# Kernel optimization log

Hardware: AMD Instinct MI355X
Metric: run time of the kernel (lower is better)

## Reference

```python
import jax, jax.numpy as jnp
import numpy as np

LST = 64  # sparsemax frame length over time


def sparsemax(z):
    """Sparsemax over the last axis (Martins & Astudillo 2016)."""
    d = z.shape[-1]
    z_sorted = jnp.flip(jnp.sort(z, axis=-1), axis=-1)           # descending
    z_cumsum = jnp.cumsum(z_sorted, axis=-1)
    k = jnp.arange(1, d + 1, dtype=z.dtype)
    support = (1.0 + k * z_sorted) > z_cumsum                    # bool, [..., d]
    k_z = jnp.sum(support, axis=-1, keepdims=True)               # int, >=1
    tau_sum = jnp.take_along_axis(z_cumsum, k_z - 1, axis=-1)
    tau = (tau_sum - 1.0) / k_z.astype(z.dtype)
    return jnp.maximum(z - tau, 0.0)


def setup_inputs() -> dict:
    key = jax.random.key(0)
    midis_out = jax.random.normal(key, (16, 11, 65536), dtype=jnp.float32)
    return {"midis_out": midis_out}


def reference(midis_out):
    batch, n_insts, time = midis_out.shape
    lst = LST
    len_pad = (lst - time % lst) % lst
    x = jnp.pad(midis_out, ((0, 0), (0, 0), (0, len_pad)))
    t_pad = time + len_pad
    # sparsemax over instruments: (b, t, i) -> sparsemax over i -> back to (b, i, t)
    out_inst = jnp.swapaxes(sparsemax(jnp.swapaxes(x, 1, 2)), 1, 2)
    # sparsemax over fixed time blocks of length lst
    out_time = sparsemax(x.reshape(batch, n_insts, t_pad // lst, lst))
    out_time = out_time.reshape(batch, n_insts, t_pad)
    return out_inst[:, :, :time] * out_time[:, :, :time]
```

## Files before the change

### kernel.cpp

```cpp
#include <hip/hip_runtime.h>

#define B_   16
#define NI   11
#define T_   65536
#define LST  64
#define NBLK (T_ / LST)
#define ROWP 68

#define DPP_XOR1 0xB1
#define DPP_XOR2 0x4E

__device__ __forceinline__ float frcp(float x) { return __builtin_amdgcn_rcpf(x); }

template<int CTRL>
__device__ __forceinline__ float dppf(float x) {
    return __int_as_float(__builtin_amdgcn_update_dpp(
        0, __float_as_int(x), CTRL, 0xF, 0xF, true));
}
template<int CTRL>
__device__ __forceinline__ int dppi(int x) {
    return __builtin_amdgcn_update_dpp(0, x, CTRL, 0xF, 0xF, true);
}

__device__ __forceinline__ void ce_desc(float& a, float& b) {
    float mx = fmaxf(a, b);
    float mn = fminf(a, b);
    a = mx; b = mn;
}

__global__ __launch_bounds__(256) void fused_sparsemax_kernel(
        const float* __restrict__ in, float* __restrict__ out) {
    __shared__ float ldsz[4][NI * ROWP];
    __shared__ float ldsti[4][64];

    const int lane = threadIdx.x & 63;
    const int wid  = threadIdx.x >> 6;
    const int tile = blockIdx.x * 4 + wid;
    const int b    = tile >> 10;
    const int jb   = tile & (NBLK - 1);

    const float* px = in + (size_t)b * NI * T_ + (size_t)jb * LST + (size_t)lane;

    float z[NI];
#pragma unroll
    for (int i = 0; i < NI; ++i) z[i] = px[(size_t)i * T_];

#pragma unroll
    for (int i = 0; i < NI; ++i) ldsz[wid][i * ROWP + lane] = z[i];

    const int g   = lane >> 2;
    const int q   = lane & 3;
    const int row = (g < NI) ? g : (g - NI);

    float y[16];
#pragma unroll
    for (int r = 0; r < 16; ++r) y[r] = ldsz[wid][row * ROWP + q * 16 + r];

    float s[NI];
#pragma unroll
    for (int i = 0; i < NI; ++i) s[i] = z[i];
#pragma unroll
    for (int p = 0; p < NI; ++p) {
#pragma unroll
        for (int k = (p & 1); k + 1 < NI; k += 2) ce_desc(s[k], s[k + 1]);
    }
    float cum = 0.0f, tsum = 0.0f;
    int   kz  = 0;
#pragma unroll
    for (int k = 1; k <= NI; ++k) {
        cum += s[k - 1];
        bool cond = fmaf((float)k, s[k - 1], 1.0f) > cum;
        kz   += cond ? 1 : 0;
        tsum += cond ? s[k - 1] : 0.0f;
    }
    const float tau_i = (tsum - 1.0f) * frcp((float)kz);
    ldsti[wid][lane] = tau_i;

    float m = y[0];
#pragma unroll
    for (int r = 1; r < 16; ++r) m = fmaxf(m, y[r]);
    m = fmaxf(m, dppf<DPP_XOR1>(m));
    m = fmaxf(m, dppf<DPP_XOR2>(m));

    float tau  = m - 1.0f;
    int   prev = 0;
#pragma unroll
    for (int it = 0; it < 3; ++it) {
        float ss = 0.0f;
        int   cc = 0;
#pragma unroll
        for (int r = 0; r < 16; ++r) {
            bool a = y[r] > tau;
            ss += a ? y[r] : 0.0f;
            cc += a ? 1 : 0;
        }
        ss += dppf<DPP_XOR1>(ss);
        ss += dppf<DPP_XOR2>(ss);
        cc += dppi<DPP_XOR1>(cc);
        cc += dppi<DPP_XOR2>(cc);
        tau  = (ss - 1.0f) * frcp((float)cc);
        prev = cc;
    }
    for (int it = 0; it < LST; ++it) {
        float ss = 0.0f;
        int   cc = 0;
#pragma unroll
        for (int r = 0; r < 16; ++r) {
            bool a = y[r] > tau;
            ss += a ? y[r] : 0.0f;
            cc += a ? 1 : 0;
        }
        cc += dppi<DPP_XOR1>(cc);
        cc += dppi<DPP_XOR2>(cc);
        if (!__any(cc != prev)) break;
        ss += dppf<DPP_XOR1>(ss);
        ss += dppf<DPP_XOR2>(ss);
        prev = cc;
        tau  = (ss - 1.0f) * frcp((float)cc);
    }

    if (g < NI) {
        float ti[16];
#pragma unroll
        for (int r = 0; r < 16; ++r) ti[r] = ldsti[wid][q * 16 + r];

        float* po = out + (size_t)b * NI * T_ + (size_t)g * T_
                        + (size_t)jb * LST + (size_t)q * 16;
        float4* po4 = reinterpret_cast<float4*>(po);
#pragma unroll
        for (int v = 0; v < 4; ++v) {
            float4 o;
            o.x = fmaxf(y[4*v+0] - tau, 0.0f) * fmaxf(y[4*v+0] - ti[4*v+0], 0.0f);
            o.y = fmaxf(y[4*v+1] - tau, 0.0f) * fmaxf(y[4*v+1] - ti[4*v+1], 0.0f);
            o.z = fmaxf(y[4*v+2] - tau, 0.0f) * fmaxf(y[4*v+2] - ti[4*v+2], 0.0f);
            o.w = fmaxf(y[4*v+3] - tau, 0.0f) * fmaxf(y[4*v+3] - ti[4*v+3], 0.0f);
            po4[v] = o;
        }
    }
}

extern "C" void kernel_launch(void* const* d_in, const int* in_sizes, int n_in,
                              void* d_out, int out_size, void* d_ws, size_t ws_size,
                              hipStream_t stream) {
    const float* in = (const float*)d_in[0];
    float* out = (float*)d_out;
    hipLaunchKernelGGL(fused_sparsemax_kernel, dim3(4096), dim3(256), 0, stream,
                       in, out);
}
```

Baseline: 28.50 us.

## Restructure into 704-thread super-tiles with one wave per instrument row

Each block now handles 1024 time steps for all 11 instruments, with one wave per instrument row. Each lane loads 16 contiguous floats as float4 vectors, so no lanes sit idle (the old layout left 20 of 64 lanes unused in the store phase). The instrument-axis sparsemax is computed per column from a shared LDS tile across the whole block, and the time-block threshold starts from a tighter initial guess to cut iterations. The cost is block-wide syncthreads, 1024 large blocks that may limit occupancy, and a possible bank-conflict pattern when reading the LDS columns.

```diff
diff --git a/kernel.cpp b/kernel.cpp
--- a/kernel.cpp
+++ b/kernel.cpp
@@ -1,11 +1,11 @@
 #include <hip/hip_runtime.h>
 
-#define B_   16
-#define NI   11
-#define T_   65536
-#define LST  64
-#define NBLK (T_ / LST)
-#define ROWP 68
+#define B_    16
+#define NI    11
+#define T_    65536
+#define LST   64
+#define SUPER 1024
+#define RSTR  1040
 
 #define DPP_XOR1 0xB1
 #define DPP_XOR2 0x4E
@@ -28,37 +28,10 @@
     a = mx; b = mn;
 }
 
-__global__ __launch_bounds__(256) void fused_sparsemax_kernel(
-        const float* __restrict__ in, float* __restrict__ out) {
-    __shared__ float ldsz[4][NI * ROWP];
-    __shared__ float ldsti[4][64];
-
-    const int lane = threadIdx.x & 63;
-    const int wid  = threadIdx.x >> 6;
-    const int tile = blockIdx.x * 4 + wid;
-    const int b    = tile >> 10;
-    const int jb   = tile & (NBLK - 1);
-
-    const float* px = in + (size_t)b * NI * T_ + (size_t)jb * LST + (size_t)lane;
-
-    float z[NI];
-#pragma unroll
-    for (int i = 0; i < NI; ++i) z[i] = px[(size_t)i * T_];
-
-#pragma unroll
-    for (int i = 0; i < NI; ++i) ldsz[wid][i * ROWP + lane] = z[i];
-
-    const int g   = lane >> 2;
-    const int q   = lane & 3;
-    const int row = (g < NI) ? g : (g - NI);
-
-    float y[16];
-#pragma unroll
-    for (int r = 0; r < 16; ++r) y[r] = ldsz[wid][row * ROWP + q * 16 + r];
-
+__device__ __forceinline__ float col_tau(float (*ldsz)[RSTR], int c) {
     float s[NI];
 #pragma unroll
-    for (int i = 0; i < NI; ++i) s[i] = z[i];
+    for (int i = 0; i < NI; ++i) s[i] = ldsz[i][c];
 #pragma unroll
     for (int p = 0; p < NI; ++p) {
 #pragma unroll
@@ -73,17 +46,47 @@
         kz   += cond ? 1 : 0;
         tsum += cond ? s[k - 1] : 0.0f;
     }
-    const float tau_i = (tsum - 1.0f) * frcp((float)kz);
-    ldsti[wid][lane] = tau_i;
+    return (tsum - 1.0f) * frcp((float)kz);
+}
 
-    float m = y[0];
+__global__ __launch_bounds__(704) void fused_sparsemax_kernel(
+        const float* __restrict__ in, float* __restrict__ out) {
+    __shared__ float ldsz[NI][RSTR];
+    __shared__ float ldsti[SUPER];
+
+    const int tid  = threadIdx.x;
+    const int lane = tid & 63;
+    const int w    = tid >> 6;
+    const int b    = blockIdx.x >> 6;
+    const int st   = blockIdx.x & 63;
+
+    const size_t rbase = ((size_t)b * NI + w) * T_ + (size_t)st * SUPER
+                       + (size_t)lane * 16;
+
+    const float4* p4 = reinterpret_cast<const float4*>(in + rbase);
+    float4 v0 = p4[0], v1 = p4[1], v2 = p4[2], v3 = p4[3];
+    float y[16] = {v0.x, v0.y, v0.z, v0.w, v1.x, v1.y, v1.z, v1.w,
+                   v2.x, v2.y, v2.z, v2.w, v3.x, v3.y, v3.z, v3.w};
+
+    float4* wp = reinterpret_cast<float4*>(&ldsz[w][lane * 16]);
+    wp[0] = v0; wp[1] = v1; wp[2] = v2; wp[3] = v3;
+    __syncthreads();
+
+    ldsti[tid] = col_tau(ldsz, tid);
+    if (tid < SUPER - 704) {
+        ldsti[tid + 704] = col_tau(ldsz, tid + 704);
+    }
+
+    float lm = y[0];
 #pragma unroll
-    for (int r = 1; r < 16; ++r) m = fmaxf(m, y[r]);
-    m = fmaxf(m, dppf<DPP_XOR1>(m));
-    m = fmaxf(m, dppf<DPP_XOR2>(m));
+    for (int r = 1; r < 16; ++r) lm = fmaxf(lm, y[r]);
+    float M1 = fmaxf(lm, dppf<DPP_XOR1>(lm));
+    M1 = fmaxf(M1, dppf<DPP_XOR2>(M1));
+    float S4 = lm + dppf<DPP_XOR1>(lm);
+    S4 += dppf<DPP_XOR2>(S4);
+    float tau  = fmaxf(M1 - 1.0f, (S4 - 1.0f) * 0.25f);
+    int   prev = 0;
 
-    float tau  = m - 1.0f;
-    int   prev = 0;
 #pragma unroll
     for (int it = 0; it < 3; ++it) {
         float ss = 0.0f;
@@ -119,23 +122,21 @@
         tau  = (ss - 1.0f) * frcp((float)cc);
     }
 
-    if (g < NI) {
-        float ti[16];
+    __syncthreads();
+
+    float ti[16];
 #pragma unroll
-        for (int r = 0; r < 16; ++r) ti[r] = ldsti[wid][q * 16 + r];
+    for (int r = 0; r < 16; ++r) ti[r] = ldsti[lane * 16 + r];
 
-        float* po = out + (size_t)b * NI * T_ + (size_t)g * T_
-                        + (size_t)jb * LST + (size_t)q * 16;
-        float4* po4 = reinterpret_cast<float4*>(po);
+    float4* po4 = reinterpret_cast<float4*>(out + rbase);
 #pragma unroll
-        for (int v = 0; v < 4; ++v) {
-            float4 o;
-            o.x = fmaxf(y[4*v+0] - tau, 0.0f) * fmaxf(y[4*v+0] - ti[4*v+0], 0.0f);
-            o.y = fmaxf(y[4*v+1] - tau, 0.0f) * fmaxf(y[4*v+1] - ti[4*v+1], 0.0f);
-            o.z = fmaxf(y[4*v+2] - tau, 0.0f) * fmaxf(y[4*v+2] - ti[4*v+2], 0.0f);
-            o.w = fmaxf(y[4*v+3] - tau, 0.0f) * fmaxf(y[4*v+3] - ti[4*v+3], 0.0f);
-            po4[v] = o;
-        }
+    for (int v = 0; v < 4; ++v) {
+        float4 o;
+        o.x = fmaxf(y[4*v+0] - tau, 0.0f) * fmaxf(y[4*v+0] - ti[4*v+0], 0.0f);
+        o.y = fmaxf(y[4*v+1] - tau, 0.0f) * fmaxf(y[4*v+1] - ti[4*v+1], 0.0f);
+        o.z = fmaxf(y[4*v+2] - tau, 0.0f) * fmaxf(y[4*v+2] - ti[4*v+2], 0.0f);
+        o.w = fmaxf(y[4*v+3] - tau, 0.0f) * fmaxf(y[4*v+3] - ti[4*v+3], 0.0f);
+        po4[v] = o;
     }
 }
 
@@ -144,6 +145,6 @@
                               hipStream_t stream) {
     const float* in = (const float*)d_in[0];
     float* out = (float*)d_out;
-    hipLaunchKernelGGL(fused_sparsemax_kernel, dim3(4096), dim3(256), 0, stream,
+    hipLaunchKernelGGL(fused_sparsemax_kernel, dim3(1024), dim3(704), 0, stream,
                        in, out);
 }
```

After: 31.61 us. 1.11x slower.
